# Performance work log

Hardware: AMD Instinct MI355X
Metric: run time of the kernel (lower is better)

Reference implementation:

```python
import jax, jax.numpy as jnp
import numpy as np

B, D = 16384, 512          # batch, outer_dim
S = R = O = X = Y = Z = 64  # inner tensor-network ranks


def _xavier(key, shape):
    fan_in, fan_out = shape[-2], shape[-1]
    if len(shape) == 3:
        fan_in = shape[0] * shape[1]
        fan_out = shape[2]
    limit = float(np.sqrt(6.0 / (fan_in + fan_out)))
    return jax.random.uniform(key, shape, jnp.float32, -limit, limit)


def setup_inputs() -> dict:
    key = jax.random.key(0)
    ks = jax.random.split(key, 12)
    return {
        "input1": jax.random.normal(ks[0], (B, D), jnp.float32),
        "input2": jax.random.normal(ks[1], (B, D), jnp.float32),
        "input3": jax.random.normal(ks[2], (B, D), jnp.float32),
        "proj_s": _xavier(ks[3], (D, S)),
        "proj_r": _xavier(ks[4], (R, R)),   # first_param = inn_r since with_nn
        "proj_o": _xavier(ks[5], (D, O)),
        "cube_s": _xavier(ks[6], (S, Y, Z)),
        "cube_r": _xavier(ks[7], (X, R, Z)),
        "cube_o": _xavier(ks[8], (X, Y, O)),
        "W21": _xavier(ks[9], (R, D)),
        "b21": jnp.zeros((R,), jnp.float32),
        "W22": _xavier(ks[10], (R, R)),
        "b22": jnp.zeros((R,), jnp.float32),
        "W23": _xavier(ks[11], (R, R)),
        "b23": jnp.zeros((R,), jnp.float32),
    }


def reference(input1, input2, input3, proj_s, proj_r, proj_o,
              cube_s, cube_r, cube_o, W21, b21, W22, b22, W23, b23):
    # relation MLP (with_nn=True branch)
    h = jax.nn.relu(input2 @ W21.T + b21)
    h = jax.nn.relu(h @ W22.T + b22)
    h = h @ W23.T + b23
    # projections: einsum('Ss,bS->bs', proj, x) == x @ proj
    p1 = input1 @ proj_s   # [B, S]
    p2 = h @ proj_r        # [B, R]
    p3 = input3 @ proj_o   # [B, O]
    # triangle contraction 'bs,br,bo,syz,xrz,xyo->b', contracted efficiently
    a = jnp.einsum('bs,syz->byz', p1, cube_s)
    b = jnp.einsum('br,xrz->bxz', p2, cube_r)
    c = jnp.einsum('bo,xyo->bxy', p3, cube_o)
    return jnp.einsum('byz,bxz,bxy->b', a, b, c)
```

## Files before the change

### kernel.cpp

```cpp
#include <hip/hip_runtime.h>
#include <hip/hip_bf16.h>
#include <cstdint>
#include <cstddef>


typedef __attribute__((ext_vector_type(8))) short short8;
typedef __attribute__((ext_vector_type(4))) float f32x4;

#define DEV static __device__ __forceinline__

constexpr int NB = 16384;
constexpr int ND = 512;

DEV unsigned short f2bf(float f) {
    union { float f; unsigned u; } v; v.f = f;
    unsigned r = v.u + 0x7FFFu + ((v.u >> 16) & 1u);
    return (unsigned short)(r >> 16);
}
DEV float bf2f(unsigned short h) {
    union { unsigned u; float f; } v; v.u = ((unsigned)h) << 16;
    return v.f;
}
DEV unsigned pack2(float lo, float hi) {
    return (unsigned)f2bf(lo) | ((unsigned)f2bf(hi) << 16);
}
DEV short8 ldA_f32(const float* p) {
    float4 a = *(const float4*)p, b = *(const float4*)(p + 4);
    union { unsigned u[4]; short8 s; } v;
    v.u[0] = pack2(a.x, a.y); v.u[1] = pack2(a.z, a.w);
    v.u[2] = pack2(b.x, b.y); v.u[3] = pack2(b.z, b.w);
    return v.s;
}

__global__ void k_prep(const float* __restrict__ proj_s, const float* __restrict__ proj_r,
                       const float* __restrict__ proj_o, const float* __restrict__ cube_o,
                       const float* __restrict__ W21, const float* __restrict__ W22,
                       const float* __restrict__ W23,
                       unsigned short* __restrict__ Wp1t, unsigned short* __restrict__ Wh1,
                       unsigned short* __restrict__ Wp3t, unsigned short* __restrict__ W22b,
                       unsigned short* __restrict__ W23b, unsigned short* __restrict__ Prt,
                       unsigned short* __restrict__ cot)
{
    int i = blockIdx.x * 256 + threadIdx.x;
    if (i < 32768) { int d = i >> 6, s = i & 63; Wp1t[s * 512 + d] = f2bf(proj_s[i]); return; }
    i -= 32768;
    if (i < 32768) { Wh1[i] = f2bf(W21[i]); return; }
    i -= 32768;
    if (i < 32768) { int d = i >> 6, o = i & 63; Wp3t[o * 512 + d] = f2bf(proj_o[i]); return; }
    i -= 32768;
    if (i < 4096) { W22b[i] = f2bf(W22[i]); return; }
    i -= 4096;
    if (i < 4096) { W23b[i] = f2bf(W23[i]); return; }
    i -= 4096;
    if (i < 4096) { int k = i >> 6, n = i & 63; Prt[n * 64 + k] = f2bf(proj_r[i]); return; }
    i -= 4096;
    if (i < 262144) { int x = i >> 12, y = (i >> 6) & 63, o = i & 63;
                      cot[o * 4096 + x * 64 + y] = f2bf(cube_o[i]); return; }
}

__global__ __launch_bounds__(256, 2) void k_F(
    const float* __restrict__ cr, const float* __restrict__ cs,
    unsigned short* __restrict__ F2)
{
    const int t = threadIdx.x, wid = t >> 6, l = t & 63, lr = l & 15, lk = l >> 4;
    const int wm = wid & 1, wn = wid >> 1;
    const int m0 = blockIdx.x * 128 + wm * 64, n0 = blockIdx.y * 128 + wn * 64;
    f32x4 acc[4][4] = {};
#pragma unroll
    for (int ks = 0; ks < 2; ++ks) {
        short8 av[4], bv[4];
#pragma unroll
        for (int f = 0; f < 4; ++f) {
            av[f] = ldA_f32(cr + (size_t)(m0 + f * 16 + lr) * 64 + ks * 32 + lk * 8);
            bv[f] = ldA_f32(cs + (size_t)(n0 + f * 16 + lr) * 64 + ks * 32 + lk * 8);
        }
#pragma unroll
        for (int f = 0; f < 4; ++f)
#pragma unroll
            for (int g = 0; g < 4; ++g)
                acc[f][g] = __builtin_amdgcn_mfma_f32_16x16x32_bf16(av[f], bv[g], acc[f][g], 0, 0, 0);
    }
#pragma unroll
    for (int f = 0; f < 4; ++f)
#pragma unroll
        for (int g = 0; g < 4; ++g)
#pragma unroll
            for (int q = 0; q < 4; ++q)
                F2[(size_t)(m0 + f * 16 + lk * 4 + q) * 4096 + n0 + g * 16 + lr] = f2bf(acc[f][g][q]);
}

DEV void mlp_mm(const unsigned short* slab_w, const unsigned short* __restrict__ W,
                int lr, int lk, f32x4 acc[4])
{
#pragma unroll
    for (int ks = 0; ks < 2; ++ks) {
        short8 av = *(const short8*)((const char*)slab_w +
                      (lr * 128 + ((ks * 64 + lk * 16) ^ ((lr & 7) << 4))));
#pragma unroll
        for (int g = 0; g < 4; ++g) {
            short8 bv = *(const short8*)(W + (g * 16 + lr) * 64 + ks * 32 + lk * 8);
            acc[g] = __builtin_amdgcn_mfma_f32_16x16x32_bf16(av, bv, acc[g], 0, 0, 0);
        }
    }
}
DEV void store_slab(unsigned short* slab_w, int lr, int lk, const f32x4 acc[4],
                    const float* __restrict__ bias, bool relu_)
{
#pragma unroll
    for (int g = 0; g < 4; ++g) {
        float bcol = bias ? bias[g * 16 + lr] : 0.0f;
#pragma unroll
        for (int q = 0; q < 4; ++q) {
            int r = lk * 4 + q, c = g * 16 + lr;
            float v = acc[g][q] + bcol;
            if (relu_) v = fmaxf(v, 0.0f);
            *(unsigned short*)((char*)slab_w + (r * 128 + ((c * 2) ^ ((r & 7) << 4)))) = f2bf(v);
        }
    }
}

__global__ __launch_bounds__(256, 2) void k_proj(
    const float* __restrict__ in1, const float* __restrict__ in2, const float* __restrict__ in3,
    const unsigned short* __restrict__ Wp1t, const unsigned short* __restrict__ Wh1,
    const unsigned short* __restrict__ Wp3t,
    const unsigned short* __restrict__ W22b, const unsigned short* __restrict__ W23b,
    const unsigned short* __restrict__ Prt,
    const float* __restrict__ b21, const float* __restrict__ b22, const float* __restrict__ b23,
    unsigned short* __restrict__ p1bf, unsigned short* __restrict__ p2bf,
    unsigned short* __restrict__ p3bf)
{
    __shared__ __align__(16) unsigned short slab[4][1024];
    const int z = blockIdx.y;
    const float* in = (z == 0) ? in1 : (z == 1) ? in2 : in3;
    const unsigned short* Wt = (z == 0) ? Wp1t : (z == 1) ? Wh1 : Wp3t;
    const int t = threadIdx.x, wid = t >> 6, l = t & 63, lr = l & 15, lk = l >> 4;
    const int rbase = blockIdx.x * 64 + wid * 16;
    const float* arow = in + (size_t)(rbase + lr) * ND;

    f32x4 acc[4] = {};
#pragma unroll
    for (int kc = 0; kc < 8; ++kc) {
#pragma unroll
        for (int ks = 0; ks < 2; ++ks) {
            short8 av = ldA_f32(arow + kc * 64 + ks * 32 + lk * 8);
#pragma unroll
            for (int g = 0; g < 4; ++g) {
                short8 bv = *(const short8*)(Wt + (size_t)(g * 16 + lr) * 512 + kc * 64 + ks * 32 + lk * 8);
                acc[g] = __builtin_amdgcn_mfma_f32_16x16x32_bf16(av, bv, acc[g], 0, 0, 0);
            }
        }
    }
    if (z != 1) {
        unsigned short* outp = (z == 0) ? p1bf : p3bf;
#pragma unroll
        for (int g = 0; g < 4; ++g)
#pragma unroll
            for (int q = 0; q < 4; ++q)
                outp[(size_t)(rbase + lk * 4 + q) * 64 + g * 16 + lr] = f2bf(acc[g][q]);
    } else {
        unsigned short* slw = slab[wid];
        store_slab(slw, lr, lk, acc, b21, true);
        __syncthreads();
        f32x4 a2[4] = {}; mlp_mm(slw, W22b, lr, lk, a2);
        store_slab(slw, lr, lk, a2, b22, true);
        __syncthreads();
        f32x4 a3[4] = {}; mlp_mm(slw, W23b, lr, lk, a3);
        store_slab(slw, lr, lk, a3, b23, false);
        __syncthreads();
        f32x4 a4[4] = {}; mlp_mm(slw, Prt, lr, lk, a4);
#pragma unroll
        for (int g = 0; g < 4; ++g)
#pragma unroll
            for (int q = 0; q < 4; ++q)
                p2bf[(size_t)(rbase + lk * 4 + q) * 64 + g * 16 + lr] = f2bf(a4[g][q]);
    }
}

__global__ __launch_bounds__(256, 2) void k_T(
    const unsigned short* __restrict__ F2, const unsigned short* __restrict__ cot,
    float* __restrict__ Tf)
{
    __shared__ float red[4][4096];
    const int s = blockIdx.x, xh = blockIdx.y;
    const int t = threadIdx.x, wid = t >> 6, l = t & 63, lr = l & 15, lk = l >> 4;
    f32x4 acc[4][4] = {};
#pragma unroll
    for (int xi = 0; xi < 4; ++xi) {
        int x = xh * 16 + wid * 4 + xi;
#pragma unroll
        for (int ks = 0; ks < 2; ++ks) {
            short8 av[4], bv[4];
#pragma unroll
            for (int f = 0; f < 4; ++f) {
                av[f] = *(const short8*)(F2 + (size_t)(x * 64 + f * 16 + lr) * 4096 + s * 64 + ks * 32 + lk * 8);
                bv[f] = *(const short8*)(cot + (size_t)(f * 16 + lr) * 4096 + x * 64 + ks * 32 + lk * 8);
            }
#pragma unroll
            for (int f = 0; f < 4; ++f)
#pragma unroll
                for (int g = 0; g < 4; ++g)
                    acc[f][g] = __builtin_amdgcn_mfma_f32_16x16x32_bf16(av[f], bv[g], acc[f][g], 0, 0, 0);
        }
    }
#pragma unroll
    for (int f = 0; f < 4; ++f)
#pragma unroll
        for (int g = 0; g < 4; ++g)
#pragma unroll
            for (int q = 0; q < 4; ++q)
                red[wid][(f * 16 + lk * 4 + q) * 64 + g * 16 + lr] = acc[f][g][q];
    __syncthreads();
#pragma unroll
    for (int i = 0; i < 16; ++i) {
        int idx = t + i * 256;
        atomicAdd(&Tf[(size_t)s * 4096 + idx],
                  red[0][idx] + red[1][idx] + red[2][idx] + red[3][idx]);
    }
}

__global__ void k_cast(const float* __restrict__ Tf, unsigned short* __restrict__ Tts)
{
    int i = blockIdx.x * 256 + threadIdx.x;
#pragma unroll
    for (int j = 0; j < 4; ++j) {
        int e = i * 4 + j;
        int s = e >> 12, k = e & 4095;
        int kc = k >> 6, kloc = k & 63;
        Tts[kc * 4096 + s * 64 + kloc] = f2bf(Tf[e]);
    }
}

__global__ __launch_bounds__(256, 4) void k_main(
    const unsigned short* __restrict__ p1bf, const unsigned short* __restrict__ p2bf,
    const unsigned short* __restrict__ p3bf, const unsigned short* __restrict__ Tts,
    float* __restrict__ out)
{
    __shared__ __align__(16) unsigned short tb[2][4096];
    const int t = threadIdx.x, wid = t >> 6, l = t & 63, lr = l & 15, lk = l >> 4;
    const int b0 = blockIdx.x * 64, kh = blockIdx.y;
    const int row = b0 + wid * 16 + lr;

    float p3v[2][8];
#pragma unroll
    for (int ks = 0; ks < 2; ++ks) {
        short8 v = *(const short8*)(p3bf + (size_t)row * 64 + ks * 32 + lk * 8);
#pragma unroll
        for (int j = 0; j < 8; ++j) p3v[ks][j] = bf2f((unsigned short)v[j]);
    }
    short8 p2r[2];
#pragma unroll
    for (int i = 0; i < 2; ++i)
        p2r[i] = *(const short8*)(p2bf + (size_t)row * 64 + kh * 16 + i * 8);

    const int srow_st = t >> 2, kb_st = (t & 3) * 32;
    const unsigned swz0 = (unsigned)(kb_st ^ ((srow_st & 7) << 4));
    const unsigned swz1 = (unsigned)((kb_st + 16) ^ ((srow_st & 7) << 4));

    {
        const uint4* src = (const uint4*)((const char*)(Tts + (size_t)(kh * 16) * 4096) + t * 32);
        uint4 v0 = src[0], v1 = src[1];
        char* dst = (char*)tb[0] + srow_st * 128;
        *(uint4*)(dst + swz0) = v0;
        *(uint4*)(dst + swz1) = v1;
        __syncthreads();
    }

    f32x4 acc[4] = {};
#pragma unroll
    for (int i = 0; i < 16; ++i) {
        const int buf = i & 1;
        uint4 n0 = {}, n1 = {};
        if (i < 15) {
            const uint4* src = (const uint4*)((const char*)(Tts + (size_t)(kh * 16 + i + 1) * 4096) + t * 32);
            n0 = src[0]; n1 = src[1];
        }
        float p2s = bf2f((unsigned short)p2r[i >> 3][i & 7]);
#pragma unroll
        for (int ks = 0; ks < 2; ++ks) {
            union { unsigned u[4]; short8 s; } a;
#pragma unroll
            for (int jj = 0; jj < 4; ++jj)
                a.u[jj] = pack2(p2s * p3v[ks][jj * 2], p2s * p3v[ks][jj * 2 + 1]);
#pragma unroll
            for (int g = 0; g < 4; ++g) {
                int n = g * 16 + lr;
                short8 bv = *(const short8*)((const char*)tb[buf] +
                              (n * 128 + ((ks * 64 + lk * 16) ^ ((n & 7) << 4))));
                acc[g] = __builtin_amdgcn_mfma_f32_16x16x32_bf16(a.s, bv, acc[g], 0, 0, 0);
            }
        }
        if (i < 15) {
            char* dst = (char*)tb[buf ^ 1] + srow_st * 128;
            *(uint4*)(dst + swz0) = n0;
            *(uint4*)(dst + swz1) = n1;
            __syncthreads();
        }
    }

    float rsum[4] = {};
#pragma unroll
    for (int g = 0; g < 4; ++g)
#pragma unroll
        for (int q = 0; q < 4; ++q) {
            int r = b0 + wid * 16 + lk * 4 + q, c = g * 16 + lr;
            rsum[q] += acc[g][q] * bf2f(p1bf[(size_t)r * 64 + c]);
        }
#pragma unroll
    for (int q = 0; q < 4; ++q) {
        float v = rsum[q];
        v += __shfl_xor(v, 1);
        v += __shfl_xor(v, 2);
        v += __shfl_xor(v, 4);
        v += __shfl_xor(v, 8);
        if (lr == 0)
            atomicAdd(&out[b0 + wid * 16 + lk * 4 + q], v);
    }
}

extern "C" void kernel_launch(void* const* d_in, const int* in_sizes, int n_in,
                              void* d_out, int out_size, void* d_ws, size_t ws_size,
                              hipStream_t stream)
{
    const float* in1    = (const float*)d_in[0];
    const float* in2    = (const float*)d_in[1];
    const float* in3    = (const float*)d_in[2];
    const float* proj_s = (const float*)d_in[3];
    const float* proj_r = (const float*)d_in[4];
    const float* proj_o = (const float*)d_in[5];
    const float* cube_s = (const float*)d_in[6];
    const float* cube_r = (const float*)d_in[7];
    const float* cube_o = (const float*)d_in[8];
    const float* W21    = (const float*)d_in[9];
    const float* b21    = (const float*)d_in[10];
    const float* W22    = (const float*)d_in[11];
    const float* b22    = (const float*)d_in[12];
    const float* W23    = (const float*)d_in[13];
    const float* b23    = (const float*)d_in[14];
    float* out = (float*)d_out;

    char* ws = (char*)d_ws;
    size_t off = 0;
    auto alloc = [&](size_t bytes) -> char* {
        char* p = ws + off;
        off += (bytes + 255) & ~(size_t)255;
        return p;
    };
    unsigned short* p1bf = (unsigned short*)alloc((size_t)NB * 64 * 2);
    unsigned short* p2bf = (unsigned short*)alloc((size_t)NB * 64 * 2);
    unsigned short* p3bf = (unsigned short*)alloc((size_t)NB * 64 * 2);
    unsigned short* Wp1t = (unsigned short*)alloc(64 * 512 * 2);
    unsigned short* Wh1  = (unsigned short*)alloc(64 * 512 * 2);
    unsigned short* Wp3t = (unsigned short*)alloc(64 * 512 * 2);
    unsigned short* W22b = (unsigned short*)alloc(64 * 64 * 2);
    unsigned short* W23b = (unsigned short*)alloc(64 * 64 * 2);
    unsigned short* Prt  = (unsigned short*)alloc(64 * 64 * 2);
    unsigned short* cot  = (unsigned short*)alloc(262144 * 2);
    float*          Tf   = (float*)alloc(262144 * 4);
    unsigned short* Tts  = (unsigned short*)alloc(262144 * 2);
    unsigned short* F2   = (unsigned short*)alloc((size_t)4096 * 4096 * 2);

    hipMemsetAsync(d_out, 0, (size_t)out_size * sizeof(float), stream);
    hipMemsetAsync(Tf, 0, 262144 * sizeof(float), stream);

    k_prep<<<1456, 256, 0, stream>>>(proj_s, proj_r, proj_o, cube_o, W21, W22, W23,
                                     Wp1t, Wh1, Wp3t, W22b, W23b, Prt, cot);
    k_F<<<dim3(32, 32), 256, 0, stream>>>(cube_r, cube_s, F2);
    k_proj<<<dim3(NB / 64, 3), 256, 0, stream>>>(in1, in2, in3, Wp1t, Wh1, Wp3t,
                                                 W22b, W23b, Prt, b21, b22, b23,
                                                 p1bf, p2bf, p3bf);
    k_T<<<dim3(64, 4), 256, 0, stream>>>(F2, cot, Tf);
    k_cast<<<256, 256, 0, stream>>>(Tf, Tts);
    k_main<<<dim3(NB / 64, 4), 256, 0, stream>>>(p1bf, p2bf, p3bf, Tts, out);
}
```

Measured before the change: 228.9 us.

## Re-layout F tensor, drop atomics/cast in k_T, stage k_proj inputs via LDS

```diff
diff --git a/kernel.cpp b/kernel.cpp
--- a/kernel.cpp
+++ b/kernel.cpp
@@ -60,7 +60,7 @@
 
 __global__ __launch_bounds__(256, 2) void k_F(
     const float* __restrict__ cr, const float* __restrict__ cs,
-    unsigned short* __restrict__ F2)
+    unsigned short* __restrict__ F3)
 {
     const int t = threadIdx.x, wid = t >> 6, l = t & 63, lr = l & 15, lk = l >> 4;
     const int wm = wid & 1, wn = wid >> 1;
@@ -80,13 +80,15 @@
             for (int g = 0; g < 4; ++g)
                 acc[f][g] = __builtin_amdgcn_mfma_f32_16x16x32_bf16(av[f], bv[g], acc[f][g], 0, 0, 0);
     }
+    const int xg = m0 >> 6, sg = n0 >> 6;
 #pragma unroll
     for (int f = 0; f < 4; ++f)
 #pragma unroll
         for (int g = 0; g < 4; ++g)
 #pragma unroll
             for (int q = 0; q < 4; ++q)
-                F2[(size_t)(m0 + f * 16 + lk * 4 + q) * 4096 + n0 + g * 16 + lr] = f2bf(acc[f][g][q]);
+                F3[(size_t)sg * 262144 + (size_t)xg * 4096 +
+                   (f * 16 + lk * 4 + q) * 64 + g * 16 + lr] = f2bf(acc[f][g][q]);
 }
 
 DEV void mlp_mm(const unsigned short* slab_w, const unsigned short* __restrict__ W,
@@ -119,7 +121,7 @@
     }
 }
 
-__global__ __launch_bounds__(256, 2) void k_proj(
+__global__ __launch_bounds__(256, 3) void k_proj(
     const float* __restrict__ in1, const float* __restrict__ in2, const float* __restrict__ in3,
     const unsigned short* __restrict__ Wp1t, const unsigned short* __restrict__ Wh1,
     const unsigned short* __restrict__ Wp3t,
@@ -129,27 +131,59 @@
     unsigned short* __restrict__ p1bf, unsigned short* __restrict__ p2bf,
     unsigned short* __restrict__ p3bf)
 {
+    __shared__ __align__(16) unsigned short at[2][64 * 128];
     __shared__ __align__(16) unsigned short slab[4][1024];
     const int z = blockIdx.y;
     const float* in = (z == 0) ? in1 : (z == 1) ? in2 : in3;
     const unsigned short* Wt = (z == 0) ? Wp1t : (z == 1) ? Wh1 : Wp3t;
     const int t = threadIdx.x, wid = t >> 6, l = t & 63, lr = l & 15, lk = l >> 4;
-    const int rbase = blockIdx.x * 64 + wid * 16;
-    const float* arow = in + (size_t)(rbase + lr) * ND;
-
+    const int b0 = blockIdx.x * 64;
+
+    const int srow = t >> 5, sc4 = t & 31;
+    const float* sbase = in + (size_t)(b0 + srow) * ND + sc4 * 4;
+    const unsigned wb0 = (unsigned)(srow * 256 + ((sc4 * 8) ^ ((srow & 7) << 4)));
+
+    float4 rg[8];
+    auto load_chunk = [&](int kc) {
+#pragma unroll
+        for (int i = 0; i < 8; ++i)
+            rg[i] = *(const float4*)(sbase + (size_t)i * 8 * ND + kc * 128);
+    };
+    auto write_chunk = [&](int buf) {
+        char* base = (char*)at[buf] + wb0;
+#pragma unroll
+        for (int i = 0; i < 8; ++i) {
+            uint2 pk;
+            pk.x = pack2(rg[i].x, rg[i].y);
+            pk.y = pack2(rg[i].z, rg[i].w);
+            *(uint2*)(base + i * 2048) = pk;
+        }
+    };
+
+    load_chunk(0);
+    write_chunk(0);
+    __syncthreads();
+
+    const int arow = wid * 16 + lr;
+    const unsigned rsw = (unsigned)((arow & 7) << 4);
     f32x4 acc[4] = {};
-#pragma unroll
-    for (int kc = 0; kc < 8; ++kc) {
-#pragma unroll
-        for (int ks = 0; ks < 2; ++ks) {
-            short8 av = ldA_f32(arow + kc * 64 + ks * 32 + lk * 8);
+    for (int kc = 0; kc < 4; ++kc) {
+        if (kc < 3) load_chunk(kc + 1);
+        const char* rb = (const char*)at[kc & 1] + arow * 256;
+#pragma unroll
+        for (int ks = 0; ks < 4; ++ks) {
+            short8 av = *(const short8*)(rb + ((unsigned)(ks * 64 + lk * 16) ^ rsw));
 #pragma unroll
             for (int g = 0; g < 4; ++g) {
-                short8 bv = *(const short8*)(Wt + (size_t)(g * 16 + lr) * 512 + kc * 64 + ks * 32 + lk * 8);
+                short8 bv = *(const short8*)(Wt + (size_t)(g * 16 + lr) * 512 + kc * 128 + ks * 32 + lk * 8);
                 acc[g] = __builtin_amdgcn_mfma_f32_16x16x32_bf16(av, bv, acc[g], 0, 0, 0);
             }
         }
-    }
+        if (kc < 3) write_chunk((kc + 1) & 1);
+        __syncthreads();
+    }
+
+    const int rbase = b0 + wid * 16;
     if (z != 1) {
         unsigned short* outp = (z == 0) ? p1bf : p3bf;
 #pragma unroll
@@ -176,57 +210,40 @@
     }
 }
 
-__global__ __launch_bounds__(256, 2) void k_T(
-    const unsigned short* __restrict__ F2, const unsigned short* __restrict__ cot,
-    float* __restrict__ Tf)
-{
-    __shared__ float red[4][4096];
-    const int s = blockIdx.x, xh = blockIdx.y;
+__global__ __launch_bounds__(256, 1) void k_T(
+    const unsigned short* __restrict__ F3, const unsigned short* __restrict__ cot,
+    unsigned short* __restrict__ Tts)
+{
+    __shared__ float red[4][1024];
+    const int s = blockIdx.x, rq = blockIdx.y;
     const int t = threadIdx.x, wid = t >> 6, l = t & 63, lr = l & 15, lk = l >> 4;
-    f32x4 acc[4][4] = {};
-#pragma unroll
-    for (int xi = 0; xi < 4; ++xi) {
-        int x = xh * 16 + wid * 4 + xi;
+    const unsigned short* Fs = F3 + (size_t)s * 262144 + (rq * 16 + lr) * 64;
+    f32x4 acc[4] = {};
+#pragma unroll
+    for (int xi = 0; xi < 16; ++xi) {
+        int x = wid * 16 + xi;
 #pragma unroll
         for (int ks = 0; ks < 2; ++ks) {
-            short8 av[4], bv[4];
-#pragma unroll
-            for (int f = 0; f < 4; ++f) {
-                av[f] = *(const short8*)(F2 + (size_t)(x * 64 + f * 16 + lr) * 4096 + s * 64 + ks * 32 + lk * 8);
-                bv[f] = *(const short8*)(cot + (size_t)(f * 16 + lr) * 4096 + x * 64 + ks * 32 + lk * 8);
+            short8 av = *(const short8*)(Fs + (size_t)x * 4096 + ks * 32 + lk * 8);
+#pragma unroll
+            for (int g = 0; g < 4; ++g) {
+                short8 bv = *(const short8*)(cot + (size_t)(g * 16 + lr) * 4096 + x * 64 + ks * 32 + lk * 8);
+                acc[g] = __builtin_amdgcn_mfma_f32_16x16x32_bf16(av, bv, acc[g], 0, 0, 0);
             }
-#pragma unroll
-            for (int f = 0; f < 4; ++f)
-#pragma unroll
-                for (int g = 0; g < 4; ++g)
-                    acc[f][g] = __builtin_amdgcn_mfma_f32_16x16x32_bf16(av[f], bv[g], acc[f][g], 0, 0, 0);
-        }
-    }
-#pragma unroll
-    for (int f = 0; f < 4; ++f)
-#pragma unroll
-        for (int g = 0; g < 4; ++g)
-#pragma unroll
-            for (int q = 0; q < 4; ++q)
-                red[wid][(f * 16 + lk * 4 + q) * 64 + g * 16 + lr] = acc[f][g][q];
+        }
+    }
+#pragma unroll
+    for (int g = 0; g < 4; ++g)
+#pragma unroll
+        for (int q = 0; q < 4; ++q)
+            red[wid][(lk * 4 + q) * 64 + g * 16 + lr] = acc[g][q];
     __syncthreads();
 #pragma unroll
-    for (int i = 0; i < 16; ++i) {
+    for (int i = 0; i < 4; ++i) {
         int idx = t + i * 256;
-        atomicAdd(&Tf[(size_t)s * 4096 + idx],
-                  red[0][idx] + red[1][idx] + red[2][idx] + red[3][idx]);
-    }
-}
-
-__global__ void k_cast(const float* __restrict__ Tf, unsigned short* __restrict__ Tts)
-{
-    int i = blockIdx.x * 256 + threadIdx.x;
-#pragma unroll
-    for (int j = 0; j < 4; ++j) {
-        int e = i * 4 + j;
-        int s = e >> 12, k = e & 4095;
-        int kc = k >> 6, kloc = k & 63;
-        Tts[kc * 4096 + s * 64 + kloc] = f2bf(Tf[e]);
+        int r_loc = idx >> 6, o = idx & 63;
+        float v = red[0][idx] + red[1][idx] + red[2][idx] + red[3][idx];
+        Tts[(size_t)(rq * 16 + r_loc) * 4096 + s * 64 + o] = f2bf(v);
     }
 }
 
@@ -355,20 +372,17 @@
     unsigned short* W23b = (unsigned short*)alloc(64 * 64 * 2);
     unsigned short* Prt  = (unsigned short*)alloc(64 * 64 * 2);
     unsigned short* cot  = (unsigned short*)alloc(262144 * 2);
-    float*          Tf   = (float*)alloc(262144 * 4);
     unsigned short* Tts  = (unsigned short*)alloc(262144 * 2);
-    unsigned short* F2   = (unsigned short*)alloc((size_t)4096 * 4096 * 2);
+    unsigned short* F3   = (unsigned short*)alloc((size_t)4096 * 4096 * 2);
 
     hipMemsetAsync(d_out, 0, (size_t)out_size * sizeof(float), stream);
-    hipMemsetAsync(Tf, 0, 262144 * sizeof(float), stream);
 
     k_prep<<<1456, 256, 0, stream>>>(proj_s, proj_r, proj_o, cube_o, W21, W22, W23,
                                      Wp1t, Wh1, Wp3t, W22b, W23b, Prt, cot);
-    k_F<<<dim3(32, 32), 256, 0, stream>>>(cube_r, cube_s, F2);
+    k_F<<<dim3(32, 32), 256, 0, stream>>>(cube_r, cube_s, F3);
     k_proj<<<dim3(NB / 64, 3), 256, 0, stream>>>(in1, in2, in3, Wp1t, Wh1, Wp3t,
                                                  W22b, W23b, Prt, b21, b22, b23,
                                                  p1bf, p2bf, p3bf);
-    k_T<<<dim3(64, 4), 256, 0, stream>>>(F2, cot, Tf);
-    k_cast<<<256, 256, 0, stream>>>(Tf, Tts);
+    k_T<<<dim3(64, 4), 256, 0, stream>>>(F3, cot, Tts);
     k_main<<<dim3(NB / 64, 4), 256, 0, stream>>>(p1bf, p2bf, p3bf, Tts, out);
 }
```

Result: no change. 228.9 us (+0.0%).
